# Kernel tuning notes

Hardware: AMD Instinct MI355X
Metric: run time of the kernel (lower is better)

## Reference

```python
import jax, jax.numpy as jnp
import numpy as np

B, S, D = 4, 2048, 64
H = 16            # num_heads
HD = D // H       # head_dim = 4 (code's misnamed 'num_heads' variable)
EPS = 1e-5        # BatchNorm1d default eps


def setup_inputs() -> dict:
    key = jax.random.key(0)
    ks = jax.random.split(key, 8)
    sc = 1.0 / np.sqrt(D)
    return {
        "x": jax.random.normal(ks[0], (B, S, D), dtype=jnp.float32),
        "Wq": jax.random.normal(ks[1], (D, D), dtype=jnp.float32) * sc,
        "bq": jnp.zeros((D,), dtype=jnp.float32),
        "Wk": jax.random.normal(ks[2], (D, D), dtype=jnp.float32) * sc,
        "bk": jnp.zeros((D,), dtype=jnp.float32),
        "Wv": jax.random.normal(ks[3], (D, D), dtype=jnp.float32) * sc,
        "bv": jnp.zeros((D,), dtype=jnp.float32),
        "gamma": jnp.ones((D,), dtype=jnp.float32),
        "beta": jnp.zeros((D,), dtype=jnp.float32),
    }


def reference(x, Wq, bq, Wk, bk, Wv, bv, gamma, beta):
    # ReLU-activated QKV projections
    Q = jax.nn.relu(jnp.einsum("bsd,de->bse", x, Wq) + bq)
    K = jax.nn.relu(jnp.einsum("bsd,de->bse", x, Wk) + bk)
    V = jax.nn.relu(jnp.einsum("bsd,de->bse", x, Wv) + bv)

    # split(dim=2)->cat(dim=0) is equivalent to head-split reshape [B,S,H,HD]
    Qh = Q.reshape(B, S, H, HD)
    Kh = K.reshape(B, S, H, HD)
    Vh = V.reshape(B, S, H, HD)

    scores = jnp.einsum("bqhd,bkhd->bhqk", Qh, Kh) / jnp.sqrt(jnp.float32(HD))
    attn = jax.nn.softmax(scores, axis=-1)  # dropout_rate = 0.0 -> no-op
    out = jnp.einsum("bhqk,bkhd->bqhd", attn, Vh).reshape(B, S, D)

    # residual
    out = out + x

    # BatchNorm1d(64) in training mode: batch stats over (B, S) per channel
    mean = jnp.mean(out, axis=(0, 1))
    var = jnp.var(out, axis=(0, 1))  # biased variance, as used for normalization
    out = (out - mean) * jax.lax.rsqrt(var + EPS) * gamma + beta
    return out
```

## Files before the change

kernel.cpp:

```cpp
#include <hip/hip_runtime.h>

#define BB 4
#define SS 2048
#define DD 64
#define HH 16
#define HDD 4
#define NBH (BB*HH)
#define NROWS (BB*SS)
#define NQ (NBH*SS)
#define QTILES 8
#define LOG2E_HALF 0.7213475204444817f

typedef float f32x2 __attribute__((ext_vector_type(2)));

__global__ __launch_bounds__(256) void qkv_kernel(
    const float* __restrict__ x,
    const float* __restrict__ Wq, const float* __restrict__ bq,
    const float* __restrict__ Wk, const float* __restrict__ bk,
    const float* __restrict__ Wv, const float* __restrict__ bv,
    float* __restrict__ Q, float* __restrict__ KV)
{
    __shared__ float xs[4 * 64];
    const int tid = threadIdx.x;
    const int row0 = blockIdx.x * 4;

    xs[tid] = x[(size_t)row0 * 64 + tid];
    __syncthreads();

    const int r = tid >> 6;
    const int c = tid & 63;
    const int row = row0 + r;
    const int b = row / SS;
    const int s = row % SS;
    const float* xr = &xs[r * 64];

    float aq = bq[c], ak = bk[c], av = bv[c];
    #pragma unroll 16
    for (int k = 0; k < 64; ++k) {
        const float xv = xr[k];
        aq = fmaf(xv, Wq[k * 64 + c], aq);
        ak = fmaf(xv, Wk[k * 64 + c], ak);
        av = fmaf(xv, Wv[k * 64 + c], av);
    }
    aq = fmaxf(aq, 0.0f);
    ak = fmaxf(ak, 0.0f) * LOG2E_HALF;
    av = fmaxf(av, 0.0f);

    const int h = c >> 2, hd = c & 3;
    const size_t bhs = ((size_t)(b * HH + h) * SS + s);
    Q[bhs * 4 + hd] = aq;

    const int p = s >> 1, po = s & 1;
    const size_t pb = ((size_t)(b * HH + h) * (SS / 2) + p) * 16;
    KV[pb + hd * 2 + po] = ak;
    KV[pb + 8 + hd * 2 + po] = av;
}

template<int KSPLIT, int QROWS, bool DIRECT>
__global__ __launch_bounds__(256) void attn_kernel(
    const float* __restrict__ Qb, const float* __restrict__ KVb,
    const float* __restrict__ x, float* __restrict__ y,
    float* __restrict__ accS, float* __restrict__ sumS)
{
    constexpr int QT = SS / (256 * QROWS);
    const int tid = threadIdx.x;
    int blk = blockIdx.x;
    const int ks = blk / (NBH * QT);
    blk -= ks * (NBH * QT);
    const int bh = blk / QT;
    const int qt = blk - bh * QT;

    const int PAIRS = SS / 2 / KSPLIT;
    const f32x2* kv = (const f32x2*)(KVb + ((size_t)bh * (SS / 2) + (size_t)ks * PAIRS) * 16);

    f32x2 qx[QROWS], qy[QROWS], qz[QROWS], qw[QROWS];
    #pragma unroll
    for (int r = 0; r < QROWS; ++r) {
        const int qrow = qt * (256 * QROWS) + r * 256 + tid;
        const float4 q = ((const float4*)Qb)[(size_t)bh * SS + qrow];
        qx[r] = {q.x, q.x}; qy[r] = {q.y, q.y};
        qz[r] = {q.z, q.z}; qw[r] = {q.w, q.w};
    }

    f32x2 acx[QROWS], acy[QROWS], acz[QROWS], acw[QROWS], sm[QROWS];
    #pragma unroll
    for (int r = 0; r < QROWS; ++r) {
        acx[r] = {0.f, 0.f}; acy[r] = {0.f, 0.f};
        acz[r] = {0.f, 0.f}; acw[r] = {0.f, 0.f};
        sm[r] = {0.f, 0.f};
    }

    #pragma unroll 2
    for (int j = 0; j < PAIRS; ++j) {
        const f32x2 kx = kv[j * 8 + 0];
        const f32x2 ky = kv[j * 8 + 1];
        const f32x2 kz = kv[j * 8 + 2];
        const f32x2 kw = kv[j * 8 + 3];
        const f32x2 vx = kv[j * 8 + 4];
        const f32x2 vy = kv[j * 8 + 5];
        const f32x2 vz = kv[j * 8 + 6];
        const f32x2 vw = kv[j * 8 + 7];
        #pragma unroll
        for (int r = 0; r < QROWS; ++r) {
            f32x2 s = qx[r] * kx;
            s = __builtin_elementwise_fma(qy[r], ky, s);
            s = __builtin_elementwise_fma(qz[r], kz, s);
            s = __builtin_elementwise_fma(qw[r], kw, s);
            f32x2 e;
            e.x = __builtin_amdgcn_exp2f(s.x);
            e.y = __builtin_amdgcn_exp2f(s.y);
            sm[r] += e;
            acx[r] = __builtin_elementwise_fma(e, vx, acx[r]);
            acy[r] = __builtin_elementwise_fma(e, vy, acy[r]);
            acz[r] = __builtin_elementwise_fma(e, vz, acz[r]);
            acw[r] = __builtin_elementwise_fma(e, vw, acw[r]);
        }
    }

    #pragma unroll
    for (int r = 0; r < QROWS; ++r) {
        const int qrow = qt * (256 * QROWS) + r * 256 + tid;
        const float sum = sm[r].x + sm[r].y;
        float4 acc = {acx[r].x + acx[r].y, acy[r].x + acy[r].y,
                      acz[r].x + acz[r].y, acw[r].x + acw[r].y};
        if (DIRECT) {
            const float inv = 1.0f / sum;
            const int b = bh >> 4, h = bh & 15;
            const size_t o = ((size_t)(b * SS + qrow)) * DD + h * HDD;
            const float4 xr = *(const float4*)(x + o);
            float4 out;
            out.x = fmaf(acc.x, inv, xr.x);
            out.y = fmaf(acc.y, inv, xr.y);
            out.z = fmaf(acc.z, inv, xr.z);
            out.w = fmaf(acc.w, inv, xr.w);
            *(float4*)(y + o) = out;
        } else {
            const size_t qi = (size_t)ks * NQ + (size_t)bh * SS + qrow;
            ((float4*)accS)[qi] = acc;
            sumS[qi] = sum;
        }
    }
}

template<int KSPLIT>
__global__ __launch_bounds__(256) void combine_bn(
    const float* __restrict__ accS, const float* __restrict__ sumS,
    const float* __restrict__ x, float* __restrict__ y,
    float* __restrict__ part2)
{
    __shared__ float r[4][8];
    const int tid = threadIdx.x;
    const int bh = blockIdx.x >> 3;
    const int qt = blockIdx.x & 7;
    const int qrow = qt * 256 + tid;
    const size_t qi = (size_t)bh * SS + qrow;

    float4 a = ((const float4*)accS)[qi];
    float s = sumS[qi];
    #pragma unroll
    for (int k = 1; k < KSPLIT; ++k) {
        const float4 a2 = ((const float4*)accS)[(size_t)k * NQ + qi];
        a.x += a2.x; a.y += a2.y; a.z += a2.z; a.w += a2.w;
        s += sumS[(size_t)k * NQ + qi];
    }
    const float inv = 1.0f / s;
    const int b = bh >> 4, h = bh & 15;
    const size_t o = ((size_t)(b * SS + qrow)) * DD + h * HDD;
    const float4 xr = *(const float4*)(x + o);
    float4 out;
    out.x = fmaf(a.x, inv, xr.x);
    out.y = fmaf(a.y, inv, xr.y);
    out.z = fmaf(a.z, inv, xr.z);
    out.w = fmaf(a.w, inv, xr.w);
    *(float4*)(y + o) = out;

    float v[8] = {out.x, out.y, out.z, out.w,
                  out.x * out.x, out.y * out.y, out.z * out.z, out.w * out.w};
    #pragma unroll
    for (int i = 0; i < 8; ++i) {
        float t = v[i];
        for (int off = 32; off > 0; off >>= 1) t += __shfl_down(t, off);
        v[i] = t;
    }
    const int wid = tid >> 6;
    if ((tid & 63) == 0) {
        #pragma unroll
        for (int i = 0; i < 8; ++i) r[wid][i] = v[i];
    }
    __syncthreads();
    if (tid < 8) {
        const float t = r[0][tid] + r[1][tid] + r[2][tid] + r[3][tid];
        const int slot = b * 8 + qt;
        const int i = tid & 3;
        const int c = h * 4 + i;
        if (tid < 4) part2[c * 32 + slot] = t;
        else         part2[2048 + c * 32 + slot] = t;
    }
}

__global__ __launch_bounds__(256) void bn_norm_fused(
    float* __restrict__ y, const float* __restrict__ part2,
    const float* __restrict__ gamma, const float* __restrict__ beta)
{
    __shared__ float st[128];
    const int tid = threadIdx.x;
    if (tid < 128) {
        const int c = tid & 63;
        const float* p = part2 + (tid >> 6) * 2048 + c * 32;
        float s = 0.f;
        #pragma unroll
        for (int i = 0; i < 32; ++i) s += p[i];
        st[tid] = s;
    }
    __syncthreads();

    const int idx = blockIdx.x * 256 + tid;
    const int c0 = (idx & 15) * 4;
    float4 v = ((const float4*)y)[idx];
    const float n = 1.0f / NROWS;
    const float m0 = st[c0] * n,     m1 = st[c0 + 1] * n;
    const float m2 = st[c0 + 2] * n, m3 = st[c0 + 3] * n;
    const float r0 = rsqrtf(st[64 + c0] * n - m0 * m0 + 1e-5f);
    const float r1 = rsqrtf(st[65 + c0] * n - m1 * m1 + 1e-5f);
    const float r2 = rsqrtf(st[66 + c0] * n - m2 * m2 + 1e-5f);
    const float r3 = rsqrtf(st[67 + c0] * n - m3 * m3 + 1e-5f);
    float4 o;
    o.x = fmaf((v.x - m0) * r0, gamma[c0],     beta[c0]);
    o.y = fmaf((v.y - m1) * r1, gamma[c0 + 1], beta[c0 + 1]);
    o.z = fmaf((v.z - m2) * r2, gamma[c0 + 2], beta[c0 + 2]);
    o.w = fmaf((v.w - m3) * r3, gamma[c0 + 3], beta[c0 + 3]);
    ((float4*)y)[idx] = o;
}

__global__ __launch_bounds__(256) void bn_reduce1(
    const float* __restrict__ y, float* __restrict__ part)
{
    __shared__ float ls[256], ls2[256];
    const int tid = threadIdx.x;
    const int c = tid & 63;
    const int rg = tid >> 6;
    const int row0 = blockIdx.x * 32 + rg * 8;
    float s = 0.0f, s2 = 0.0f;
    #pragma unroll
    for (int i = 0; i < 8; ++i) {
        const float v = y[(size_t)(row0 + i) * 64 + c];
        s += v;
        s2 = fmaf(v, v, s2);
    }
    ls[tid] = s; ls2[tid] = s2;
    __syncthreads();
    if (rg == 0) {
        part[blockIdx.x * 64 + c] = ls[c] + ls[64 + c] + ls[128 + c] + ls[192 + c];
        part[256 * 64 + blockIdx.x * 64 + c] = ls2[c] + ls2[64 + c] + ls2[128 + c] + ls2[192 + c];
    }
}

__global__ __launch_bounds__(256) void bn_reduce2(
    const float* __restrict__ part, float* __restrict__ stats)
{
    __shared__ float ls[256], ls2[256];
    const int tid = threadIdx.x;
    const int c = tid & 63;
    const int pg = tid >> 6;
    float s = 0.0f, s2 = 0.0f;
    for (int i = pg; i < 256; i += 4) {
        s  += part[i * 64 + c];
        s2 += part[256 * 64 + i * 64 + c];
    }
    ls[tid] = s; ls2[tid] = s2;
    __syncthreads();
    if (pg == 0) {
        const float ts  = ls[c]  + ls[64 + c]  + ls[128 + c]  + ls[192 + c];
        const float ts2 = ls2[c] + ls2[64 + c] + ls2[128 + c] + ls2[192 + c];
        const float mean = ts * (1.0f / NROWS);
        const float var  = ts2 * (1.0f / NROWS) - mean * mean;
        stats[c] = mean;
        stats[64 + c] = rsqrtf(var + 1e-5f);
    }
}

__global__ __launch_bounds__(256) void bn_norm(
    float* __restrict__ y, const float* __restrict__ stats,
    const float* __restrict__ gamma, const float* __restrict__ beta)
{
    const int idx = blockIdx.x * 256 + threadIdx.x;
    const int c = idx & 63;
    const float v = y[idx];
    y[idx] = fmaf((v - stats[c]) * stats[64 + c], gamma[c], beta[c]);
}

extern "C" void kernel_launch(void* const* d_in, const int* in_sizes, int n_in,
                              void* d_out, int out_size, void* d_ws, size_t ws_size,
                              hipStream_t stream)
{
    const float* x     = (const float*)d_in[0];
    const float* Wq    = (const float*)d_in[1];
    const float* bq    = (const float*)d_in[2];
    const float* Wk    = (const float*)d_in[3];
    const float* bk    = (const float*)d_in[4];
    const float* Wv    = (const float*)d_in[5];
    const float* bv    = (const float*)d_in[6];
    const float* gamma = (const float*)d_in[7];
    const float* beta  = (const float*)d_in[8];
    float* out = (float*)d_out;

    float* ws = (float*)d_ws;
    float* Q  = ws;
    float* KV = ws + 524288;

    qkv_kernel<<<NROWS / 4, 256, 0, stream>>>(x, Wq, bq, Wk, bk, Wv, bv, Q, KV);

    const size_t base = 524288 + 1048576;
    auto need = [](int kk) {
        return (size_t)(524288 + 1048576 + (size_t)kk * NQ * 5 + 4096 + 128) * 4;
    };
    constexpr int QR = 2;
    constexpr int QT = SS / (256 * QR);

    if (ws_size >= need(8)) {
        float* accS  = ws + base;
        float* sumS  = accS + (size_t)8 * NQ * 4;
        float* part2 = sumS + (size_t)8 * NQ;
        attn_kernel<8, QR, false><<<8 * NBH * QT, 256, 0, stream>>>(Q, KV, x, out, accS, sumS);
        combine_bn<8><<<NBH * QTILES, 256, 0, stream>>>(accS, sumS, x, out, part2);
        bn_norm_fused<<<NROWS * DD / 1024, 256, 0, stream>>>(out, part2, gamma, beta);
    } else if (ws_size >= need(4)) {
        float* accS  = ws + base;
        float* sumS  = accS + (size_t)4 * NQ * 4;
        float* part2 = sumS + (size_t)4 * NQ;
        attn_kernel<4, QR, false><<<4 * NBH * QT, 256, 0, stream>>>(Q, KV, x, out, accS, sumS);
        combine_bn<4><<<NBH * QTILES, 256, 0, stream>>>(accS, sumS, x, out, part2);
        bn_norm_fused<<<NROWS * DD / 1024, 256, 0, stream>>>(out, part2, gamma, beta);
    } else if (ws_size >= need(2)) {
        float* accS  = ws + base;
        float* sumS  = accS + (size_t)2 * NQ * 4;
        float* part2 = sumS + (size_t)2 * NQ;
        attn_kernel<2, QR, false><<<2 * NBH * QT, 256, 0, stream>>>(Q, KV, x, out, accS, sumS);
        combine_bn<2><<<NBH * QTILES, 256, 0, stream>>>(accS, sumS, x, out, part2);
        bn_norm_fused<<<NROWS * DD / 1024, 256, 0, stream>>>(out, part2, gamma, beta);
    } else {
        float* part  = ws + base;
        float* stats = part + 32768;
        attn_kernel<1, QR, true><<<NBH * QT, 256, 0, stream>>>(Q, KV, x, out, nullptr, nullptr);
        bn_reduce1<<<256, 256, 0, stream>>>(out, part);
        bn_reduce2<<<1, 256, 0, stream>>>(part, stats);
        bn_norm<<<NROWS * DD / 256, 256, 0, stream>>>(out, stats, gamma, beta);
    }
}
```

Before: 113.6 us.

## Fuse BN normalization into combine kernel via grid-wide atomic barrier

Merges the combine/BN-stats kernel and the BN normalize kernel into one launch. Blocks publish partial sums, then spin on a global counter (reset in the QKV kernel) until all 512 blocks arrive, and normalize their outputs in registers. This removes one kernel launch and a full write-then-reread of the output tensor. It relies on all 512 blocks being co-resident (launch_bounds 256,2), otherwise the spin barrier deadlocks. It also replaces the division and modulo in QKV with shift and mask.

```diff
diff --git a/kernel.cpp b/kernel.cpp
--- a/kernel.cpp
+++ b/kernel.cpp
@@ -9,6 +9,7 @@
 #define NROWS (BB*SS)
 #define NQ (NBH*SS)
 #define QTILES 8
+#define CNBLK (NBH*QTILES)
 #define LOG2E_HALF 0.7213475204444817f
 
 typedef float f32x2 __attribute__((ext_vector_type(2)));
@@ -18,8 +19,12 @@
     const float* __restrict__ Wq, const float* __restrict__ bq,
     const float* __restrict__ Wk, const float* __restrict__ bk,
     const float* __restrict__ Wv, const float* __restrict__ bv,
-    float* __restrict__ Q, float* __restrict__ KV)
-{
+    float* __restrict__ Q, float* __restrict__ KV,
+    unsigned int* __restrict__ counter)
+{
+    if (blockIdx.x == 0 && threadIdx.x == 0)
+        __hip_atomic_store(counter, 0u, __ATOMIC_RELAXED, __HIP_MEMORY_SCOPE_AGENT);
+
     __shared__ float xs[4 * 64];
     const int tid = threadIdx.x;
     const int row0 = blockIdx.x * 4;
@@ -30,8 +35,8 @@
     const int r = tid >> 6;
     const int c = tid & 63;
     const int row = row0 + r;
-    const int b = row / SS;
-    const int s = row % SS;
+    const int b = row >> 11;
+    const int s = row & (SS - 1);
     const float* xr = &xs[r * 64];
 
     float aq = bq[c], ak = bk[c], av = bv[c];
@@ -143,12 +148,14 @@
 }
 
 template<int KSPLIT>
-__global__ __launch_bounds__(256) void combine_bn(
+__global__ __launch_bounds__(256, 2) void combine_bn_norm(
     const float* __restrict__ accS, const float* __restrict__ sumS,
     const float* __restrict__ x, float* __restrict__ y,
-    float* __restrict__ part2)
-{
-    __shared__ float r[4][8];
+    float* __restrict__ part2, unsigned int* __restrict__ counter,
+    const float* __restrict__ gamma, const float* __restrict__ beta)
+{
+    __shared__ float rr[4][8];
+    __shared__ float st8[8];
     const int tid = threadIdx.x;
     const int bh = blockIdx.x >> 3;
     const int qt = blockIdx.x & 7;
@@ -172,7 +179,6 @@
     out.y = fmaf(a.y, inv, xr.y);
     out.z = fmaf(a.z, inv, xr.z);
     out.w = fmaf(a.w, inv, xr.w);
-    *(float4*)(y + o) = out;
 
     float v[8] = {out.x, out.y, out.z, out.w,
                   out.x * out.x, out.y * out.y, out.z * out.z, out.w * out.w};
@@ -185,51 +191,51 @@
     const int wid = tid >> 6;
     if ((tid & 63) == 0) {
         #pragma unroll
-        for (int i = 0; i < 8; ++i) r[wid][i] = v[i];
+        for (int i = 0; i < 8; ++i) rr[wid][i] = v[i];
     }
     __syncthreads();
     if (tid < 8) {
-        const float t = r[0][tid] + r[1][tid] + r[2][tid] + r[3][tid];
+        const float t = rr[0][tid] + rr[1][tid] + rr[2][tid] + rr[3][tid];
         const int slot = b * 8 + qt;
         const int i = tid & 3;
         const int c = h * 4 + i;
-        if (tid < 4) part2[c * 32 + slot] = t;
-        else         part2[2048 + c * 32 + slot] = t;
-    }
-}
-
-__global__ __launch_bounds__(256) void bn_norm_fused(
-    float* __restrict__ y, const float* __restrict__ part2,
-    const float* __restrict__ gamma, const float* __restrict__ beta)
-{
-    __shared__ float st[128];
-    const int tid = threadIdx.x;
-    if (tid < 128) {
-        const int c = tid & 63;
-        const float* p = part2 + (tid >> 6) * 2048 + c * 32;
-        float s = 0.f;
+        float* dst = (tid < 4) ? &part2[c * 32 + slot]
+                               : &part2[2048 + c * 32 + slot];
+        __hip_atomic_store(dst, t, __ATOMIC_RELAXED, __HIP_MEMORY_SCOPE_AGENT);
+    }
+    __threadfence();
+    __syncthreads();
+
+    if (tid == 0) {
+        __hip_atomic_fetch_add(counter, 1u, __ATOMIC_ACQ_REL, __HIP_MEMORY_SCOPE_AGENT);
+        while (__hip_atomic_load(counter, __ATOMIC_ACQUIRE, __HIP_MEMORY_SCOPE_AGENT) < (unsigned)CNBLK) {}
+    }
+    __syncthreads();
+
+    if (tid < 8) {
+        const int i = tid & 3;
+        const int reg = tid >> 2;
+        const float* p = part2 + reg * 2048 + (h * 4 + i) * 32;
+        float acc2 = 0.f;
         #pragma unroll
-        for (int i = 0; i < 32; ++i) s += p[i];
-        st[tid] = s;
-    }
-    __syncthreads();
-
-    const int idx = blockIdx.x * 256 + tid;
-    const int c0 = (idx & 15) * 4;
-    float4 v = ((const float4*)y)[idx];
+        for (int k = 0; k < 32; ++k)
+            acc2 += __hip_atomic_load(p + k, __ATOMIC_RELAXED, __HIP_MEMORY_SCOPE_AGENT);
+        st8[tid] = acc2;
+    }
+    __syncthreads();
+
     const float n = 1.0f / NROWS;
-    const float m0 = st[c0] * n,     m1 = st[c0 + 1] * n;
-    const float m2 = st[c0 + 2] * n, m3 = st[c0 + 3] * n;
-    const float r0 = rsqrtf(st[64 + c0] * n - m0 * m0 + 1e-5f);
-    const float r1 = rsqrtf(st[65 + c0] * n - m1 * m1 + 1e-5f);
-    const float r2 = rsqrtf(st[66 + c0] * n - m2 * m2 + 1e-5f);
-    const float r3 = rsqrtf(st[67 + c0] * n - m3 * m3 + 1e-5f);
-    float4 o;
-    o.x = fmaf((v.x - m0) * r0, gamma[c0],     beta[c0]);
-    o.y = fmaf((v.y - m1) * r1, gamma[c0 + 1], beta[c0 + 1]);
-    o.z = fmaf((v.z - m2) * r2, gamma[c0 + 2], beta[c0 + 2]);
-    o.w = fmaf((v.w - m3) * r3, gamma[c0 + 3], beta[c0 + 3]);
-    ((float4*)y)[idx] = o;
+    const int c0 = h * 4;
+    const float m0 = st8[0] * n, m1 = st8[1] * n, m2 = st8[2] * n, m3 = st8[3] * n;
+    const float r0 = rsqrtf(st8[4] * n - m0 * m0 + 1e-5f);
+    const float r1 = rsqrtf(st8[5] * n - m1 * m1 + 1e-5f);
+    const float r2 = rsqrtf(st8[6] * n - m2 * m2 + 1e-5f);
+    const float r3 = rsqrtf(st8[7] * n - m3 * m3 + 1e-5f);
+    out.x = fmaf((out.x - m0) * r0, gamma[c0],     beta[c0]);
+    out.y = fmaf((out.y - m1) * r1, gamma[c0 + 1], beta[c0 + 1]);
+    out.z = fmaf((out.z - m2) * r2, gamma[c0 + 2], beta[c0 + 2]);
+    out.w = fmaf((out.w - m3) * r3, gamma[c0 + 3], beta[c0 + 3]);
+    *(float4*)(y + o) = out;
 }
 
 __global__ __launch_bounds__(256) void bn_reduce1(
@@ -308,8 +314,6 @@
     float* Q  = ws;
     float* KV = ws + 524288;
 
-    qkv_kernel<<<NROWS / 4, 256, 0, stream>>>(x, Wq, bq, Wk, bk, Wv, bv, Q, KV);
-
     const size_t base = 524288 + 1048576;
     auto need = [](int kk) {
         return (size_t)(524288 + 1048576 + (size_t)kk * NQ * 5 + 4096 + 128) * 4;
@@ -321,26 +325,31 @@
         float* accS  = ws + base;
         float* sumS  = accS + (size_t)8 * NQ * 4;
         float* part2 = sumS + (size_t)8 * NQ;
+        unsigned int* counter = (unsigned int*)(part2 + 4096);
+        qkv_kernel<<<NROWS / 4, 256, 0, stream>>>(x, Wq, bq, Wk, bk, Wv, bv, Q, KV, counter);
         attn_kernel<8, QR, false><<<8 * NBH * QT, 256, 0, stream>>>(Q, KV, x, out, accS, sumS);
-        combine_bn<8><<<NBH * QTILES, 256, 0, stream>>>(accS, sumS, x, out, part2);
-        bn_norm_fused<<<NROWS * DD / 1024, 256, 0, stream>>>(out, part2, gamma, beta);
+        combine_bn_norm<8><<<CNBLK, 256, 0, stream>>>(accS, sumS, x, out, part2, counter, gamma, beta);
     } else if (ws_size >= need(4)) {
         float* accS  = ws + base;
         float* sumS  = accS + (size_t)4 * NQ * 4;
         float* part2 = sumS + (size_t)4 * NQ;
+        unsigned int* counter = (unsigned int*)(part2 + 4096);
+        qkv_kernel<<<NROWS / 4, 256, 0, stream>>>(x, Wq, bq, Wk, bk, Wv, bv, Q, KV, counter);
         attn_kernel<4, QR, false><<<4 * NBH * QT, 256, 0, stream>>>(Q, KV, x, out, accS, sumS);
-        combine_bn<4><<<NBH * QTILES, 256, 0, stream>>>(accS, sumS, x, out, part2);
-        bn_norm_fused<<<NROWS * DD / 1024, 256, 0, stream>>>(out, part2, gamma, beta);
+        combine_bn_norm<4><<<CNBLK, 256, 0, stream>>>(accS, sumS, x, out, part2, counter, gamma, beta);
     } else if (ws_size >= need(2)) {
         float* accS  = ws + base;
         float* sumS  = accS + (size_t)2 * NQ * 4;
         float* part2 = sumS + (size_t)2 * NQ;
+        unsigned int* counter = (unsigned int*)(part2 + 4096);
+        qkv_kernel<<<NROWS / 4, 256, 0, stream>>>(x, Wq, bq, Wk, bk, Wv, bv, Q, KV, counter);
         attn_kernel<2, QR, false><<<2 * NBH * QT, 256, 0, stream>>>(Q, KV, x, out, accS, sumS);
-        combine_bn<2><<<NBH * QTILES, 256, 0, stream>>>(accS, sumS, x, out, part2);
-        bn_norm_fused<<<NROWS * DD / 1024, 256, 0, stream>>>(out, part2, gamma, beta);
+        combine_bn_norm<2><<<CNBLK, 256, 0, stream>>>(accS, sumS, x, out, part2, counter, gamma, beta);
     } else {
         float* part  = ws + base;
         float* stats = part + 32768;
+        unsigned int* counter = (unsigned int*)(stats + 128);
+        qkv_kernel<<<NROWS / 4, 256, 0, stream>>>(x, Wq, bq, Wk, bk, Wv, bv, Q, KV, counter);
         attn_kernel<1, QR, true><<<NBH * QT, 256, 0, stream>>>(Q, KV, x, out, nullptr, nullptr);
         bn_reduce1<<<256, 256, 0, stream>>>(out, part);
         bn_reduce2<<<1, 256, 0, stream>>>(part, stats);
```

Result: slower. 166.9 us (+47.0%).
